# Kernel tuning notes

Measured on AMD Instinct MI355X. Metric: run time of the kernel, lower is better.

## Reference

```python
import jax, jax.numpy as jnp
import numpy as np

EPS = 1e-6     # vnn repo EPS used in VN nonlinearity / batchnorm norm
BN_EPS = 1e-5  # torch BatchNorm default eps
K = 40         # args.n_knn


def knn_idx(x, k):
    # x: (B, 3, N) -> (B, N, k) indices of k nearest neighbors (incl. self)
    inner = -2.0 * jnp.einsum('bdn,bdm->bnm', x, x)
    xx = jnp.sum(x * x, axis=1)  # (B, N)
    neg_dist = -xx[:, :, None] - inner - xx[:, None, :]
    _, idx = jax.lax.top_k(neg_dist, k)
    return idx


def get_graph_feature_cross(x, k):
    # x: (B, 3, N) -> (B, 3, 3, N, k): channels are [nbr - ctr, ctr, cross(nbr, ctr)]
    pts = jnp.transpose(x, (0, 2, 1))  # (B, N, 3)
    idx = knn_idx(x, k)                # (B, N, k)
    nbr = jax.vmap(lambda p, i: p[i])(pts, idx)          # (B, N, k, 3)
    ctr = jnp.broadcast_to(pts[:, :, None, :], nbr.shape)
    cross = jnp.cross(nbr, ctr)
    feat = jnp.stack([nbr - ctr, ctr, cross], axis=3)    # (B, N, k, 3, 3)
    return jnp.transpose(feat, (0, 3, 4, 1, 2))          # (B, C=3, 3vec, N, k)


def vn_bn(x):
    # VNBatchNorm (training-mode batch stats, affine = identity at init)
    # x: (B, C, 3, *rest); normalize the per-vector norm across (B, *rest)
    norm = jnp.sqrt(jnp.sum(x * x, axis=2)) + EPS  # (B, C, *rest)
    axes = (0,) + tuple(range(2, norm.ndim))
    mean = jnp.mean(norm, axis=axes, keepdims=True)
    var = jnp.var(norm, axis=axes, keepdims=True)
    norm_bn = (norm - mean) / jnp.sqrt(var + BN_EPS)
    return x / jnp.expand_dims(norm, 2) * jnp.expand_dims(norm_bn, 2)


def vn_lin(W, x):
    # channel-wise linear on axis 1 of (B, C, 3, ...)
    return jnp.einsum('oc,bc...->bo...', W, x)


def vn_lrelu(x, Wf, Wd):
    # VNLinearLeakyReLU with negative_slope=0.0
    p = vn_bn(vn_lin(Wf, x))
    d = vn_lin(Wd, x)
    dot = jnp.sum(p * d, axis=2, keepdims=True)
    dsq = jnp.sum(d * d, axis=2, keepdims=True)
    neg = p - (dot / (dsq + EPS)) * d  # project out the d component
    return jnp.where(dot >= 0, p, neg)


def vn_max_pool(x, W):
    # pool over last axis, picking the element maximizing <x, d> per (B, C, n)
    d = vn_lin(W, x)
    dot = jnp.sum(x * d, axis=2, keepdims=True)          # (B, C, 1, ..., K)
    idx = jnp.argmax(dot, axis=-1, keepdims=True)        # (B, C, 1, ..., 1)
    idx = jnp.broadcast_to(idx, x.shape[:-1] + (1,))
    return jnp.take_along_axis(x, idx, axis=-1)[..., 0]


def setup_inputs() -> dict:
    key = jax.random.key(0)
    ks = jax.random.split(key, 16)
    def w(k, o, i):
        bound = 1.0 / np.sqrt(i)  # torch nn.Linear default init
        return jax.random.uniform(k, (o, i), jnp.float32, -bound, bound)
    B, N = 8, 2048
    C1, C2, C3 = 64 // 3, 128 // 3, 1024 // 3  # 21, 42, 341
    F1, F2 = 512 // 3, 256 // 3                # 170, 85
    return {
        'x': jax.random.normal(ks[0], (B, 3, N), jnp.float32),
        'W_pos_feat': w(ks[1], C1, 3), 'W_pos_dir': w(ks[2], C1, 3),
        'W_gpool': w(ks[3], C1, C1),
        'W1_feat': w(ks[4], C1, C1), 'W1_dir': w(ks[5], C1, C1),
        'W2_feat': w(ks[6], C2, C1), 'W2_dir': w(ks[7], C2, C1),
        'W3_feat': w(ks[8], C3, C2), 'W3_dir': w(ks[9], C3, C2),
        'W_pool': w(ks[10], C3, C3),
        'Wf1_feat': w(ks[11], F1, C3), 'Wf1_dir': w(ks[12], F1, C3),
        'Wf2_feat': w(ks[13], F2, F1), 'Wf2_dir': w(ks[14], F2, F1),
        'Wf3': w(ks[15], 3, F2),
    }


def reference(x, W_pos_feat, W_pos_dir, W_gpool, W1_feat, W1_dir, W2_feat, W2_dir,
              W3_feat, W3_dir, W_pool, Wf1_feat, Wf1_dir, Wf2_feat, Wf2_dir, Wf3):
    feat = get_graph_feature_cross(x, K)            # (B, 3, 3, N, K)
    h = vn_lrelu(feat, W_pos_feat, W_pos_dir)       # (B, 21, 3, N, K)
    h = vn_max_pool(h, W_gpool)                     # (B, 21, 3, N)
    h = vn_lrelu(h, W1_feat, W1_dir)                # (B, 21, 3, N)
    h = vn_lrelu(h, W2_feat, W2_dir)                # (B, 42, 3, N)
    h = vn_lrelu(h, W3_feat, W3_dir)                # (B, 341, 3, N)
    h = vn_max_pool(h, W_pool)                      # (B, 341, 3)
    h = vn_lrelu(h, Wf1_feat, Wf1_dir)              # (B, 170, 3)
    h = vn_lrelu(h, Wf2_feat, Wf2_dir)              # (B, 85, 3)
    return vn_lin(Wf3, h)                           # (B, 3, 3)
```

## Files before the change

kernel.cpp:

```cpp
#include <hip/hip_runtime.h>

#define NP 2048
#define BATCH 8
#define KNN 40
#define EPSF 1e-6f
#define BNEPS 1e-5f

typedef __attribute__((ext_vector_type(8))) short short8;
typedef __attribute__((ext_vector_type(4))) float f32x4;

__device__ __forceinline__ unsigned ordf(float v){
  unsigned u = __float_as_uint(v);
  return (u & 0x80000000u) ? ~u : (u | 0x80000000u);
}

__device__ __forceinline__ void bsplit(float v, unsigned short &h, unsigned short &l){
  unsigned u = __float_as_uint(v);
  unsigned hu = (u + 0x7fffu + ((u >> 16) & 1u)) >> 16;
  h = (unsigned short)hu;
  float r = v - __uint_as_float(hu << 16);
  unsigned u2 = __float_as_uint(r);
  l = (unsigned short)((u2 + 0x7fffu + ((u2 >> 16) & 1u)) >> 16);
}

__device__ __forceinline__ float bf2f(unsigned short h){
  return __uint_as_float(((unsigned)h) << 16);
}

__global__ __launch_bounds__(256) void knn_kernel(const float* __restrict__ x, int* __restrict__ idx){
  __shared__ float4 sP[NP];
  int tid = threadIdx.x;
  int w = tid >> 6, lane = tid & 63;
  int row = blockIdx.x * 4 + w;
  int b = row >> 11, i = row & 2047;
  const float* xb = x + b * 3 * NP;
  for (int t = tid; t < NP; t += 256){
    float a = xb[t], c = xb[NP + t], d = xb[2*NP + t];
    float xx = __fadd_rn(__fadd_rn(__fmul_rn(a,a), __fmul_rn(c,c)), __fmul_rn(d,d));
    sP[t] = make_float4(a, c, d, xx);
  }
  __syncthreads();
  float4 pi = sP[i];
  const float4* lp = &sP[lane];
  unsigned long long s0 = 0, s1 = 0, s2 = 0, s3 = 0;
  #pragma unroll
  for (int m = 0; m < 32; m++){
    float4 pj = lp[m * 64];
    float dot = __fadd_rn(__fadd_rn(__fmul_rn(pi.x, pj.x), __fmul_rn(pi.y, pj.y)), __fmul_rn(pi.z, pj.z));
    float v = __fsub_rn(__fsub_rn(-pi.w, __fmul_rn(-2.f, dot)), pj.w);
    unsigned long long pk = ((unsigned long long)ordf(v) << 32) | (unsigned)(2047 - (m*64 + lane));
    if (pk > s3){
      if (pk > s2){ s3 = s2; if (pk > s1){ s2 = s1; if (pk > s0){ s1 = s0; s0 = pk; } else s1 = pk; } else s2 = pk; }
      else s3 = pk;
    }
  }
  unsigned myout = 0;
  unsigned long long lastPop = ~0ull;
  for (int kk = 0; kk < KNN; kk++){
    unsigned hv = (unsigned)(s0 >> 32);
    unsigned vm = hv;
    #pragma unroll
    for (int st = 32; st > 0; st >>= 1){
      unsigned o = (unsigned)__shfl_xor((int)vm, st, 64);
      vm = (o > vm) ? o : vm;
    }
    bool cand = (hv == vm);
    unsigned long long msk = __ballot(cand);
    unsigned lo;
    if (__popcll(msk) == 1){
      int wl = __ffsll((unsigned long long)msk) - 1;
      lo = (unsigned)__shfl((int)(unsigned)s0, wl, 64);
    } else {
      unsigned cl = cand ? (unsigned)s0 : 0u;
      #pragma unroll
      for (int st = 32; st > 0; st >>= 1){
        unsigned o = (unsigned)__shfl_xor((int)cl, st, 64);
        cl = (o > cl) ? o : cl;
      }
      lo = cl;
    }
    if (lane == kk) myout = lo;
    if (cand && (unsigned)s0 == lo){
      lastPop = s0;
      s0 = s1; s1 = s2; s2 = s3; s3 = 0;
      if (s0 == 0){
        unsigned long long best = 0;
        #pragma unroll
        for (int m = 0; m < 32; m++){
          float4 pj = lp[m * 64];
          float dot = __fadd_rn(__fadd_rn(__fmul_rn(pi.x, pj.x), __fmul_rn(pi.y, pj.y)), __fmul_rn(pi.z, pj.z));
          float v = __fsub_rn(__fsub_rn(-pi.w, __fmul_rn(-2.f, dot)), pj.w);
          unsigned long long pk = ((unsigned long long)ordf(v) << 32) | (unsigned)(2047 - (m*64 + lane));
          if (pk < lastPop && pk > best) best = pk;
        }
        s0 = best;
      }
    }
  }
  if (lane < KNN) idx[row * KNN + lane] = 2047 - (int)myout;
}

__global__ __launch_bounds__(256) void gf_stats(const float* __restrict__ x, const int* __restrict__ idx,
                                                const float* __restrict__ Wf, double* __restrict__ sums){
  int tid0 = blockIdx.x * 256 + threadIdx.x;
  float s[21], q[21];
  #pragma unroll
  for (int o = 0; o < 21; o++){ s[o] = 0.f; q[o] = 0.f; }
  for (int pix = tid0; pix < BATCH * NP * KNN; pix += 256 * 256){
    int rem = pix / KNN;
    int n = rem & 2047, b = rem >> 11;
    int j = idx[pix];
    const float* xb = x + b * 3 * NP;
    float c0 = xb[n], c1 = xb[NP + n], c2 = xb[2*NP + n];
    float a0 = xb[j], a1 = xb[NP + j], a2 = xb[2*NP + j];
    float r0 = a0 - c0, r1 = a1 - c1, r2 = a2 - c2;
    float g0 = a1*c2 - a2*c1, g1 = a2*c0 - a0*c2, g2 = a0*c1 - a1*c0;
    #pragma unroll
    for (int o = 0; o < 21; o++){
      float w0 = Wf[o*3], w1 = Wf[o*3+1], w2 = Wf[o*3+2];
      float p0 = w0*r0 + w1*c0 + w2*g0;
      float p1 = w0*r1 + w1*c1 + w2*g1;
      float p2 = w0*r2 + w1*c2 + w2*g2;
      float nm = sqrtf(p0*p0 + p1*p1 + p2*p2) + EPSF;
      s[o] += nm; q[o] += nm * nm;
    }
  }
  __shared__ float bs[4][42];
  int w = threadIdx.x >> 6;
  #pragma unroll
  for (int o = 0; o < 21; o++){
    float a = s[o], bb = q[o];
    #pragma unroll
    for (int st = 1; st < 64; st <<= 1){ a += __shfl_xor(a, st, 64); bb += __shfl_xor(bb, st, 64); }
    if ((threadIdx.x & 63) == 0){ bs[w][o] = a; bs[w][21 + o] = bb; }
  }
  __syncthreads();
  if (threadIdx.x < 42){
    float tot = bs[0][threadIdx.x] + bs[1][threadIdx.x] + bs[2][threadIdx.x] + bs[3][threadIdx.x];
    int o = threadIdx.x % 21, sq = threadIdx.x / 21;
    atomicAdd(&sums[2*o + sq], (double)tot);
  }
}

__global__ __launch_bounds__(256) void gf_applypool(const float* __restrict__ x, const int* __restrict__ idx,
    const float* __restrict__ Wf, const float* __restrict__ Wd, const float* __restrict__ Wg,
    const float* __restrict__ mi, float* __restrict__ h1){
  int w = threadIdx.x >> 6, lane = threadIdx.x & 63;
  int pix = blockIdx.x * 4 + w;
  int n = pix & 2047, b = pix >> 11;
  const float* xb = x + b * 3 * NP;
  float c0 = xb[n], c1 = xb[NP + n], c2 = xb[2*NP + n];
  int j = (lane < KNN) ? idx[pix * KNN + lane] : n;
  float a0 = xb[j], a1 = xb[NP + j], a2 = xb[2*NP + j];
  float r0 = a0 - c0, r1 = a1 - c1, r2 = a2 - c2;
  float g0 = a1*c2 - a2*c1, g1 = a2*c0 - a0*c2, g2 = a0*c1 - a1*c0;
  float h[21][3];
  #pragma unroll
  for (int o = 0; o < 21; o++){
    float w0 = Wf[o*3], w1 = Wf[o*3+1], w2 = Wf[o*3+2];
    float p0 = w0*r0 + w1*c0 + w2*g0;
    float p1 = w0*r1 + w1*c1 + w2*g1;
    float p2 = w0*r2 + w1*c2 + w2*g2;
    float nm = sqrtf(p0*p0 + p1*p1 + p2*p2) + EPSF;
    float f = (nm - mi[2*o]) * mi[2*o+1] / nm;
    p0 *= f; p1 *= f; p2 *= f;
    float v0 = Wd[o*3], v1 = Wd[o*3+1], v2 = Wd[o*3+2];
    float d0 = v0*r0 + v1*c0 + v2*g0;
    float d1 = v0*r1 + v1*c1 + v2*g1;
    float d2 = v0*r2 + v1*c2 + v2*g2;
    float dot = p0*d0 + p1*d1 + p2*d2;
    float dsq = d0*d0 + d1*d1 + d2*d2;
    float t = dot / (dsq + EPSF);
    h[o][0] = (dot >= 0.f) ? p0 : fmaf(-t, d0, p0);
    h[o][1] = (dot >= 0.f) ? p1 : fmaf(-t, d1, p1);
    h[o][2] = (dot >= 0.f) ? p2 : fmaf(-t, d2, p2);
  }
  #pragma unroll
  for (int o = 0; o < 21; o++){
    float q0 = 0.f, q1 = 0.f, q2 = 0.f;
    #pragma unroll
    for (int c = 0; c < 21; c++){
      float wg = Wg[o*21 + c];
      q0 = fmaf(wg, h[c][0], q0); q1 = fmaf(wg, h[c][1], q1); q2 = fmaf(wg, h[c][2], q2);
    }
    float dp = q0*h[o][0] + q1*h[o][1] + q2*h[o][2];
    float m = (lane < KNN) ? dp : -INFINITY;
    #pragma unroll
    for (int s = 32; s > 0; s >>= 1) m = fmaxf(m, __shfl_xor(m, s, 64));
    unsigned long long msk = __ballot(lane < KNN && dp == m);
    int wl = __ffsll(msk) - 1;
    float o0 = __shfl(h[o][0], wl, 64);
    float o1 = __shfl(h[o][1], wl, 64);
    float o2 = __shfl(h[o][2], wl, 64);
    if (lane == 0){
      float* dst = h1 + (size_t)((b*21 + o)*3) * NP + n;
      dst[0] = o0; dst[NP] = o1; dst[2*NP] = o2;
    }
  }
}

template<int CIN>
__global__ __launch_bounds__(256) void layer_stats2(const float* __restrict__ hin, const float* __restrict__ Wf,
                                                    double* __restrict__ sums, int Co){
  const int px0 = blockIdx.x * 1024;
  const int b = px0 >> 11;
  const int n0 = (px0 & 2047) + (threadIdx.x << 2);
  const int o0 = blockIdx.y * 8;
  const float* hb = hin + (size_t)b * CIN * 3 * NP + n0;
  float p[8][3][4];
  #pragma unroll
  for (int oo = 0; oo < 8; oo++)
    #pragma unroll
    for (int e = 0; e < 3; e++)
      #pragma unroll
      for (int k = 0; k < 4; k++) p[oo][e][k] = 0.f;
  for (int c = 0; c < CIN; c++){
    float4 hv[3];
    #pragma unroll
    for (int e = 0; e < 3; e++) hv[e] = *(const float4*)&hb[(size_t)(c*3 + e) * NP];
    #pragma unroll
    for (int oo = 0; oo < 8; oo++){
      int o = o0 + oo; if (o >= Co) o = Co - 1;
      float wv = Wf[o*CIN + c];
      #pragma unroll
      for (int e = 0; e < 3; e++){
        p[oo][e][0] = fmaf(wv, hv[e].x, p[oo][e][0]);
        p[oo][e][1] = fmaf(wv, hv[e].y, p[oo][e][1]);
        p[oo][e][2] = fmaf(wv, hv[e].z, p[oo][e][2]);
        p[oo][e][3] = fmaf(wv, hv[e].w, p[oo][e][3]);
      }
    }
  }
  float sl[8], ql[8];
  #pragma unroll
  for (int oo = 0; oo < 8; oo++){
    sl[oo] = 0.f; ql[oo] = 0.f;
    #pragma unroll
    for (int k = 0; k < 4; k++){
      float nm = sqrtf(p[oo][0][k]*p[oo][0][k] + p[oo][1][k]*p[oo][1][k] + p[oo][2][k]*p[oo][2][k]) + EPSF;
      sl[oo] += nm; ql[oo] += nm * nm;
    }
  }
  __shared__ float red[4][16];
  int w = threadIdx.x >> 6;
  #pragma unroll
  for (int oo = 0; oo < 8; oo++){
    float sv = sl[oo], qv = ql[oo];
    #pragma unroll
    for (int st = 1; st < 64; st <<= 1){ sv += __shfl_xor(sv, st, 64); qv += __shfl_xor(qv, st, 64); }
    if ((threadIdx.x & 63) == 0){ red[w][oo] = sv; red[w][8 + oo] = qv; }
  }
  __syncthreads();
  if (threadIdx.x < 16){
    float tot = red[0][threadIdx.x] + red[1][threadIdx.x] + red[2][threadIdx.x] + red[3][threadIdx.x];
    int oo = threadIdx.x & 7, isq = threadIdx.x >> 3;
    int o = o0 + oo;
    if (o < Co) atomicAdd(&sums[2*o + isq], (double)tot);
  }
}

template<int CIN>
__global__ __launch_bounds__(256) void layer_apply2(const float* __restrict__ hin, const float* __restrict__ Wf,
    const float* __restrict__ Wd, const float* __restrict__ mi, float* __restrict__ hout, int Co){
  const int px = blockIdx.x * 256 + threadIdx.x;
  const int b = px >> 11, n = px & 2047;
  const int o0 = blockIdx.y * 8;
  const float* hb = hin + (size_t)b * CIN * 3 * NP + n;
  float p[8][3], d[8][3];
  #pragma unroll
  for (int oo = 0; oo < 8; oo++)
    #pragma unroll
    for (int e = 0; e < 3; e++){ p[oo][e] = 0.f; d[oo][e] = 0.f; }
  for (int c = 0; c < CIN; c++){
    float h0 = hb[(size_t)(c*3 + 0) * NP];
    float h1 = hb[(size_t)(c*3 + 1) * NP];
    float h2 = hb[(size_t)(c*3 + 2) * NP];
    #pragma unroll
    for (int oo = 0; oo < 8; oo++){
      int o = o0 + oo; if (o >= Co) o = Co - 1;
      float wf = Wf[o*CIN + c], wd = Wd[o*CIN + c];
      p[oo][0] = fmaf(wf, h0, p[oo][0]); p[oo][1] = fmaf(wf, h1, p[oo][1]); p[oo][2] = fmaf(wf, h2, p[oo][2]);
      d[oo][0] = fmaf(wd, h0, d[oo][0]); d[oo][1] = fmaf(wd, h1, d[oo][1]); d[oo][2] = fmaf(wd, h2, d[oo][2]);
    }
  }
  #pragma unroll
  for (int oo = 0; oo < 8; oo++){
    int o = o0 + oo;
    if (o < Co){
      float nm = sqrtf(p[oo][0]*p[oo][0] + p[oo][1]*p[oo][1] + p[oo][2]*p[oo][2]) + EPSF;
      float f = (nm - mi[2*o]) * mi[2*o+1] / nm;
      float p0 = p[oo][0]*f, p1 = p[oo][1]*f, p2 = p[oo][2]*f;
      float dot = p0*d[oo][0] + p1*d[oo][1] + p2*d[oo][2];
      float dsq = d[oo][0]*d[oo][0] + d[oo][1]*d[oo][1] + d[oo][2]*d[oo][2];
      float t = dot / (dsq + EPSF);
      float r0 = (dot >= 0.f) ? p0 : fmaf(-t, d[oo][0], p0);
      float r1 = (dot >= 0.f) ? p1 : fmaf(-t, d[oo][1], p1);
      float r2 = (dot >= 0.f) ? p2 : fmaf(-t, d[oo][2], p2);
      float* dst = hout + (size_t)((b*Co + o)*3) * NP + n;
      dst[0] = r0; dst[NP] = r1; dst[2*NP] = r2;
    }
  }
}

__global__ __launch_bounds__(256) void layer_apply_l3v2(const float* __restrict__ hin, const float* __restrict__ Wf,
    const float* __restrict__ Wd, const float* __restrict__ mi,
    unsigned short* __restrict__ Hkh, unsigned short* __restrict__ Hkl){
  const int px = blockIdx.x * 256 + threadIdx.x;
  const int b = px >> 11, n = px & 2047;
  const int o0 = blockIdx.y * 8;
  const float* hb = hin + (size_t)b * 42 * 3 * NP + n;
  float r[8][3];
  #pragma unroll
  for (int oo = 0; oo < 8; oo++)
    #pragma unroll
    for (int e = 0; e < 3; e++) r[oo][e] = 0.f;
  if (o0 < 341){
    float p[8][3], d[8][3];
    #pragma unroll
    for (int oo = 0; oo < 8; oo++)
      #pragma unroll
      for (int e = 0; e < 3; e++){ p[oo][e] = 0.f; d[oo][e] = 0.f; }
    for (int c = 0; c < 42; c++){
      float h0 = hb[(size_t)(c*3 + 0) * NP];
      float h1 = hb[(size_t)(c*3 + 1) * NP];
      float h2 = hb[(size_t)(c*3 + 2) * NP];
      #pragma unroll
      for (int oo = 0; oo < 8; oo++){
        int o = o0 + oo; if (o >= 341) o = 340;
        float wf = Wf[o*42 + c], wd = Wd[o*42 + c];
        p[oo][0] = fmaf(wf, h0, p[oo][0]); p[oo][1] = fmaf(wf, h1, p[oo][1]); p[oo][2] = fmaf(wf, h2, p[oo][2]);
        d[oo][0] = fmaf(wd, h0, d[oo][0]); d[oo][1] = fmaf(wd, h1, d[oo][1]); d[oo][2] = fmaf(wd, h2, d[oo][2]);
      }
    }
    #pragma unroll
    for (int oo = 0; oo < 8; oo++){
      int o = o0 + oo;
      if (o < 341){
        float nm = sqrtf(p[oo][0]*p[oo][0] + p[oo][1]*p[oo][1] + p[oo][2]*p[oo][2]) + EPSF;
        float f = (nm - mi[2*o]) * mi[2*o+1] / nm;
        float p0 = p[oo][0]*f, p1 = p[oo][1]*f, p2 = p[oo][2]*f;
        float dot = p0*d[oo][0] + p1*d[oo][1] + p2*d[oo][2];
        float dsq = d[oo][0]*d[oo][0] + d[oo][1]*d[oo][1] + d[oo][2]*d[oo][2];
        float t = dot / (dsq + EPSF);
        r[oo][0] = (dot >= 0.f) ? p0 : fmaf(-t, d[oo][0], p0);
        r[oo][1] = (dot >= 0.f) ? p1 : fmaf(-t, d[oo][1], p1);
        r[oo][2] = (dot >= 0.f) ? p2 : fmaf(-t, d[oo][2], p2);
      }
    }
  }
  #pragma unroll
  for (int e = 0; e < 3; e++){
    unsigned ph[4], pl[4];
    #pragma unroll
    for (int oo = 0; oo < 8; oo++){
      unsigned short hh, ll;
      bsplit(r[oo][e], hh, ll);
      if (!(oo & 1)){ ph[oo>>1] = hh; pl[oo>>1] = ll; }
      else { ph[oo>>1] |= ((unsigned)hh) << 16; pl[oo>>1] |= ((unsigned)ll) << 16; }
    }
    size_t base = ((((size_t)(b*3 + e))*48 + blockIdx.y) * 2048 + n) * 8;
    *(uint4*)(Hkh + base) = make_uint4(ph[0], ph[1], ph[2], ph[3]);
    *(uint4*)(Hkl + base) = make_uint4(pl[0], pl[1], pl[2], pl[3]);
  }
}

__global__ void finalize_stats(const double* __restrict__ sums, float* __restrict__ mi, int Co, double invM){
  int o = blockIdx.x * 64 + threadIdx.x;
  if (o >= Co) return;
  double m = sums[2*o] * invM;
  double v = sums[2*o+1] * invM - m * m;
  if (v < 0.0) v = 0.0;
  mi[2*o] = (float)m;
  mi[2*o+1] = (float)(1.0 / sqrt(v + (double)BNEPS));
}

__global__ __launch_bounds__(256) void wk_kernel(const float* __restrict__ Wp,
    unsigned short* __restrict__ Wkh, unsigned short* __restrict__ Wkl){
  int t = blockIdx.x * 256 + threadIdx.x;
  if (t >= 44*384*8) return;
  int j = t & 7, o = (t >> 3) % 384, cb = t / (384*8);
  int c = cb*8 + j;
  float v = (c < 341 && o < 341) ? Wp[o*341 + c] : 0.f;
  unsigned short h, l;
  bsplit(v, h, l);
  Wkh[t] = h; Wkl[t] = l;
}

__global__ __launch_bounds__(256) void pool_mfma(const unsigned short* __restrict__ Wkh,
    const unsigned short* __restrict__ Wkl, const unsigned short* __restrict__ Hkh,
    const unsigned short* __restrict__ Hkl, unsigned long long* __restrict__ packed){
  __shared__ unsigned short sB[2][2][4][64][8];
  const int b = blockIdx.z, o0 = blockIdx.y * 128, n0 = blockIdx.x * 64;
  const int t = threadIdx.x, w = t >> 6, l = t & 63;
  const int wo = o0 + w * 32;
  const int r = l & 15, g = l >> 4;
  const int skb = t >> 6, sn = t & 63;
  const int ktw = wo >> 5;

  f32x4 acc[2][4], dotv[2][4], hval[2][4];
  #pragma unroll
  for (int s = 0; s < 2; s++)
    #pragma unroll
    for (int nt = 0; nt < 4; nt++){ dotv[s][nt] = (f32x4)0.f; hval[s][nt] = (f32x4)0.f; }

  auto gsrc = [&](const unsigned short* base, int e, int kt) -> const uint4* {
    return (const uint4*)(base + ((((size_t)(b*3 + e))*48 + (size_t)(kt*4 + skb)) * 2048 + n0 + sn) * 8);
  };

  uint4 rg[2];
  rg[0] = *gsrc(Hkh, 0, 0);
  rg[1] = *gsrc(Hkl, 0, 0);

  for (int ek = 0; ek < 33; ek++){
    const int e = ek / 11, kt = ek - e*11, buf = ek & 1;
    *(uint4*)&sB[buf][0][skb][sn][0] = rg[0];
    *(uint4*)&sB[buf][1][skb][sn][0] = rg[1];
    __syncthreads();
    if (ek < 32){
      int e2 = (ek+1) / 11, kt2 = (ek+1) - e2*11;
      rg[0] = *gsrc(Hkh, e2, kt2);
      rg[1] = *gsrc(Hkl, e2, kt2);
    }
    if (kt == 0){
      #pragma unroll
      for (int s = 0; s < 2; s++)
        #pragma unroll
        for (int nt = 0; nt < 4; nt++) acc[s][nt] = (f32x4)0.f;
    }
    short8 ah[2], al[2];
    #pragma unroll
    for (int s = 0; s < 2; s++){
      size_t aoff = (((size_t)(kt*4 + g)) * 384 + (wo + s*16 + r)) * 8;
      ah[s] = *(const short8*)(Wkh + aoff);
      al[s] = *(const short8*)(Wkl + aoff);
    }
    #pragma unroll
    for (int nt = 0; nt < 4; nt++){
      short8 bh = *(const short8*)&sB[buf][0][g][nt*16 + r][0];
      short8 bl = *(const short8*)&sB[buf][1][g][nt*16 + r][0];
      #pragma unroll
      for (int s = 0; s < 2; s++){
        acc[s][nt] = __builtin_amdgcn_mfma_f32_16x16x32_bf16(ah[s], bh, acc[s][nt], 0, 0, 0);
        acc[s][nt] = __builtin_amdgcn_mfma_f32_16x16x32_bf16(ah[s], bl, acc[s][nt], 0, 0, 0);
        acc[s][nt] = __builtin_amdgcn_mfma_f32_16x16x32_bf16(al[s], bh, acc[s][nt], 0, 0, 0);
      }
    }
    if (kt == ktw){
      #pragma unroll
      for (int s = 0; s < 2; s++){
        #pragma unroll
        for (int jj = 0; jj < 4; jj++){
          int oin = s*16 + g*4 + jj;
          #pragma unroll
          for (int nt = 0; nt < 4; nt++){
            hval[s][nt][jj] = bf2f(sB[buf][0][oin>>3][nt*16 + r][oin&7])
                            + bf2f(sB[buf][1][oin>>3][nt*16 + r][oin&7]);
          }
        }
      }
    }
    __syncthreads();
    if (kt == 10){
      #pragma unroll
      for (int s = 0; s < 2; s++)
        #pragma unroll
        for (int nt = 0; nt < 4; nt++)
          #pragma unroll
          for (int jj = 0; jj < 4; jj++)
            dotv[s][nt][jj] += acc[s][nt][jj] * hval[s][nt][jj];
    }
  }
  #pragma unroll
  for (int s = 0; s < 2; s++){
    #pragma unroll
    for (int j = 0; j < 4; j++){
      int o = wo + s*16 + g*4 + j;
      unsigned long long best = 0;
      #pragma unroll
      for (int nt = 0; nt < 4; nt++){
        int n = n0 + nt*16 + r;
        unsigned long long pk = ((unsigned long long)ordf(dotv[s][nt][j]) << 32) | (unsigned)(2047 - n);
        if (pk > best) best = pk;
      }
      #pragma unroll
      for (int st = 1; st < 16; st <<= 1){
        unsigned long long ob = __shfl_xor(best, st, 64);
        if (ob > best) best = ob;
      }
      if (r == 0 && o < 341) atomicMax(&packed[b*341 + o], best);
    }
  }
}

__global__ void pool_gather(const unsigned long long* __restrict__ packed,
                            const unsigned short* __restrict__ Hkh, const unsigned short* __restrict__ Hkl,
                            float* __restrict__ pooled){
  int t = blockIdx.x * 256 + threadIdx.x;
  if (t >= BATCH * 341) return;
  int n = 2047 - (int)(packed[t] & 0xffffffffu);
  int b = t / 341, o = t % 341;
  #pragma unroll
  for (int e = 0; e < 3; e++){
    size_t hb = ((((size_t)(b*3 + e))*48 + (o >> 3)) * 2048 + n) * 8 + (o & 7);
    pooled[t*3 + e] = bf2f(Hkh[hb]) + bf2f(Hkl[hb]);
  }
}

__global__ __launch_bounds__(64) void flayer(const float* __restrict__ in, const float* __restrict__ Wf,
    const float* __restrict__ Wd, float* __restrict__ out, int Cin, int Co){
  int o = blockIdx.x, lane = threadIdx.x;
  float pv[24], dv[24];
  #pragma unroll
  for (int be = 0; be < 24; be++){ pv[be] = 0.f; dv[be] = 0.f; }
  for (int c = lane; c < Cin; c += 64){
    float wf = Wf[o*Cin + c], wd = Wd[o*Cin + c];
    #pragma unroll
    for (int bb = 0; bb < 8; bb++){
      #pragma unroll
      for (int e = 0; e < 3; e++){
        float hv = in[(bb*Cin + c)*3 + e];
        pv[bb*3+e] = fmaf(wf, hv, pv[bb*3+e]);
        dv[bb*3+e] = fmaf(wd, hv, dv[bb*3+e]);
      }
    }
  }
  #pragma unroll
  for (int be = 0; be < 24; be++){
    #pragma unroll
    for (int st = 1; st < 64; st <<= 1){
      pv[be] += __shfl_xor(pv[be], st, 64);
      dv[be] += __shfl_xor(dv[be], st, 64);
    }
  }
  float nm[8], dotb[8], dsqb[8];
  float mean = 0.f;
  #pragma unroll
  for (int bb = 0; bb < 8; bb++){
    nm[bb] = sqrtf(pv[bb*3]*pv[bb*3] + pv[bb*3+1]*pv[bb*3+1] + pv[bb*3+2]*pv[bb*3+2]) + EPSF;
    mean += nm[bb];
  }
  mean *= 0.125f;
  float var = 0.f;
  #pragma unroll
  for (int bb = 0; bb < 8; bb++){ float dvv = nm[bb] - mean; var += dvv * dvv; }
  var *= 0.125f;
  float istd = 1.f / sqrtf(var + BNEPS);
  #pragma unroll
  for (int bb = 0; bb < 8; bb++){
    float f = (nm[bb] - mean) * istd / nm[bb];
    dotb[bb] = f * (pv[bb*3]*dv[bb*3] + pv[bb*3+1]*dv[bb*3+1] + pv[bb*3+2]*dv[bb*3+2]);
    dsqb[bb] = dv[bb*3]*dv[bb*3] + dv[bb*3+1]*dv[bb*3+1] + dv[bb*3+2]*dv[bb*3+2];
  }
  #pragma unroll
  for (int be = 0; be < 24; be++){
    if (lane == be){
      int bb = be / 3;
      float f = (nm[bb] - mean) * istd / nm[bb];
      float pe = pv[be] * f;
      float t = dotb[bb] / (dsqb[bb] + EPSF);
      float res = (dotb[bb] >= 0.f) ? pe : fmaf(-t, dv[be], pe);
      out[(bb*Co + o)*3 + (be % 3)] = res;
    }
  }
}

__global__ void final_lin(const float* __restrict__ in, const float* __restrict__ W, float* __restrict__ out){
  int t = threadIdx.x;
  if (t >= 72) return;
  int b = t / 9, o = (t % 9) / 3, e = t % 3;
  float s = 0.f;
  for (int c = 0; c < 85; c++) s = fmaf(W[o*85 + c], in[(b*85 + c)*3 + e], s);
  out[t] = s;
}

extern "C" void kernel_launch(void* const* d_in, const int* in_sizes, int n_in,
                              void* d_out, int out_size, void* d_ws, size_t ws_size,
                              hipStream_t stream){
  const float* x   = (const float*)d_in[0];
  const float* Wpf = (const float*)d_in[1];
  const float* Wpd = (const float*)d_in[2];
  const float* Wg  = (const float*)d_in[3];
  const float* W1f = (const float*)d_in[4];
  const float* W1d = (const float*)d_in[5];
  const float* W2f = (const float*)d_in[6];
  const float* W2d = (const float*)d_in[7];
  const float* W3f = (const float*)d_in[8];
  const float* W3d = (const float*)d_in[9];
  const float* Wpool = (const float*)d_in[10];
  const float* Wf1f = (const float*)d_in[11];
  const float* Wf1d = (const float*)d_in[12];
  const float* Wf2f = (const float*)d_in[13];
  const float* Wf2d = (const float*)d_in[14];
  const float* Wf3  = (const float*)d_in[15];
  float* out = (float*)d_out;

  char* ws = (char*)d_ws;
  size_t off = 0;
  int*   idx = (int*)(ws + off);              off += (size_t)BATCH*NP*KNN*4;
  float* h1  = (float*)(ws + off);            off += (size_t)BATCH*21*3*NP*4;
  float* h2  = (float*)(ws + off);            off += (size_t)BATCH*21*3*NP*4;
  float* h3  = (float*)(ws + off);            off += (size_t)BATCH*42*3*NP*4;
  unsigned short* Hkh = (unsigned short*)(ws + off); off += (size_t)BATCH*3*48*NP*8*2;
  unsigned short* Hkl = (unsigned short*)(ws + off); off += (size_t)BATCH*3*48*NP*8*2;
  unsigned short* Wkh = (unsigned short*)(ws + off); off += (size_t)44*384*8*2;
  unsigned short* Wkl = (unsigned short*)(ws + off); off += (size_t)44*384*8*2;
  char*  zbase = ws + off;
  double* sums_gf = (double*)(ws + off);      off += 8192;
  double* sums_l1 = (double*)(ws + off);      off += 8192;
  double* sums_l2 = (double*)(ws + off);      off += 8192;
  double* sums_l3 = (double*)(ws + off);      off += 8192;
  unsigned long long* packed = (unsigned long long*)(ws + off); off += 24576;
  size_t zbytes = (ws + off) - zbase;
  float* mi_gf = (float*)(ws + off);          off += 1024;
  float* mi_l1 = (float*)(ws + off);          off += 1024;
  float* mi_l2 = (float*)(ws + off);          off += 1024;
  float* mi_l3 = (float*)(ws + off);          off += 4096;
  float* pooled = (float*)(ws + off);         off += (size_t)BATCH*341*3*4 + 32;
  float* h5 = (float*)(ws + off);             off += (size_t)BATCH*170*3*4 + 32;
  float* h6 = (float*)(ws + off);             off += (size_t)BATCH*85*3*4 + 32;

  hipMemsetAsync(zbase, 0, zbytes, stream);

  knn_kernel<<<BATCH*NP/4, 256, 0, stream>>>(x, idx);
  wk_kernel<<<(44*384*8 + 255)/256, 256, 0, stream>>>(Wpool, Wkh, Wkl);

  gf_stats<<<256, 256, 0, stream>>>(x, idx, Wpf, sums_gf);
  finalize_stats<<<1, 64, 0, stream>>>(sums_gf, mi_gf, 21, 1.0 / (double)(BATCH*NP*KNN));
  gf_applypool<<<BATCH*NP/4, 256, 0, stream>>>(x, idx, Wpf, Wpd, Wg, mi_gf, h1);

  layer_stats2<21><<<dim3(16,3), 256, 0, stream>>>(h1, W1f, sums_l1, 21);
  finalize_stats<<<1, 64, 0, stream>>>(sums_l1, mi_l1, 21, 1.0 / (double)(BATCH*NP));
  layer_apply2<21><<<dim3(64,3), 256, 0, stream>>>(h1, W1f, W1d, mi_l1, h2, 21);

  layer_stats2<21><<<dim3(16,6), 256, 0, stream>>>(h2, W2f, sums_l2, 42);
  finalize_stats<<<1, 64, 0, stream>>>(sums_l2, mi_l2, 42, 1.0 / (double)(BATCH*NP));
  layer_apply2<21><<<dim3(64,6), 256, 0, stream>>>(h2, W2f, W2d, mi_l2, h3, 42);

  layer_stats2<42><<<dim3(16,43), 256, 0, stream>>>(h3, W3f, sums_l3, 341);
  finalize_stats<<<6, 64, 0, stream>>>(sums_l3, mi_l3, 341, 1.0 / (double)(BATCH*NP));
  layer_apply_l3v2<<<dim3(64,44), 256, 0, stream>>>(h3, W3f, W3d, mi_l3, Hkh, Hkl);

  pool_mfma<<<dim3(32, 3, BATCH), 256, 0, stream>>>(Wkh, Wkl, Hkh, Hkl, packed);
  pool_gather<<<(BATCH*341 + 255)/256, 256, 0, stream>>>(packed, Hkh, Hkl, pooled);

  flayer<<<170, 64, 0, stream>>>(pooled, Wf1f, Wf1d, h5, 341, 170);
  flayer<<<85, 64, 0, stream>>>(h5, Wf2f, Wf2d, h6, 170, 85);
  final_lin<<<1, 128, 0, stream>>>(h6, Wf3, out);
}
```

Before: 533.6 us.

## Restructure first-layer apply+pool to 8 threads per point with packed argmax

The first VN layer plus max-pool kernel is remapped from one wavefront per point (40 of 64 lanes active) to 8 threads per point, each handling 5 neighbours. Each thread keeps a packed (score, index) running max per channel, and the winners are reduced with three xor shuffles. Afterwards the winning neighbour's feature is recomputed rather than shuffled across lanes. This removes the idle lanes and the per-channel 64-wide reductions, at the cost of a second, transposed index array written by the knn kernel and extra recompute work per output.

```diff
diff --git a/kernel.cpp b/kernel.cpp
--- a/kernel.cpp
+++ b/kernel.cpp
@@ -27,7 +27,8 @@
   return __uint_as_float(((unsigned)h) << 16);
 }
 
-__global__ __launch_bounds__(256) void knn_kernel(const float* __restrict__ x, int* __restrict__ idx){
+__global__ __launch_bounds__(256) void knn_kernel(const float* __restrict__ x, int* __restrict__ idx,
+                                                  int* __restrict__ idxT){
   __shared__ float4 sP[NP];
   int tid = threadIdx.x;
   int w = tid >> 6, lane = tid & 63;
@@ -97,7 +98,11 @@
       }
     }
   }
-  if (lane < KNN) idx[row * KNN + lane] = 2047 - (int)myout;
+  if (lane < KNN){
+    int v = 2047 - (int)myout;
+    idx[row * KNN + lane] = v;
+    idxT[lane * (BATCH*NP) + row] = v;
+  }
 }
 
 __global__ __launch_bounds__(256) void gf_stats(const float* __restrict__ x, const int* __restrict__ idx,
@@ -142,57 +147,99 @@
   }
 }
 
-__global__ __launch_bounds__(256) void gf_applypool(const float* __restrict__ x, const int* __restrict__ idx,
+#define KSPLIT 8
+#define KPER 5
+__global__ __launch_bounds__(256) void gf_applypool2(const float* __restrict__ x, const int* __restrict__ idxT,
     const float* __restrict__ Wf, const float* __restrict__ Wd, const float* __restrict__ Wg,
     const float* __restrict__ mi, float* __restrict__ h1){
-  int w = threadIdx.x >> 6, lane = threadIdx.x & 63;
-  int pix = blockIdx.x * 4 + w;
-  int n = pix & 2047, b = pix >> 11;
+  __shared__ float4 sP[NP];
+  const int tid = threadIdx.x;
+  const int pxl = tid >> 3, kc = tid & 7;
+  const int px = blockIdx.x * 32 + pxl;
+  const int b = px >> 11, n = px & 2047;
   const float* xb = x + b * 3 * NP;
-  float c0 = xb[n], c1 = xb[NP + n], c2 = xb[2*NP + n];
-  int j = (lane < KNN) ? idx[pix * KNN + lane] : n;
-  float a0 = xb[j], a1 = xb[NP + j], a2 = xb[2*NP + j];
-  float r0 = a0 - c0, r1 = a1 - c1, r2 = a2 - c2;
-  float g0 = a1*c2 - a2*c1, g1 = a2*c0 - a0*c2, g2 = a0*c1 - a1*c0;
-  float h[21][3];
+  for (int t = tid; t < NP; t += 256){
+    sP[t] = make_float4(xb[t], xb[NP + t], xb[2*NP + t], 0.f);
+  }
+  __syncthreads();
+  float4 pc = sP[n];
+  unsigned long long bestpk[21];
+  #pragma unroll
+  for (int o = 0; o < 21; o++) bestpk[o] = 0ull;
+  #pragma unroll 1
+  for (int ki = 0; ki < KPER; ki++){
+    int kg = kc * KPER + ki;
+    int j = idxT[kg * (BATCH*NP) + px];
+    float4 pj = sP[j];
+    float r0 = pj.x - pc.x, r1 = pj.y - pc.y, r2 = pj.z - pc.z;
+    float g0 = pj.y*pc.z - pj.z*pc.y, g1 = pj.z*pc.x - pj.x*pc.z, g2 = pj.x*pc.y - pj.y*pc.x;
+    float h[21][3];
+    #pragma unroll
+    for (int o = 0; o < 21; o++){
+      float w0 = Wf[o*3], w1 = Wf[o*3+1], w2 = Wf[o*3+2];
+      float p0 = w0*r0 + w1*pc.x + w2*g0;
+      float p1 = w0*r1 + w1*pc.y + w2*g1;
+      float p2 = w0*r2 + w1*pc.z + w2*g2;
+      float nm = sqrtf(p0*p0 + p1*p1 + p2*p2) + EPSF;
+      float f = (nm - mi[2*o]) * mi[2*o+1] / nm;
+      p0 *= f; p1 *= f; p2 *= f;
+      float v0 = Wd[o*3], v1 = Wd[o*3+1], v2 = Wd[o*3+2];
+      float d0 = v0*r0 + v1*pc.x + v2*g0;
+      float d1 = v0*r1 + v1*pc.y + v2*g1;
+      float d2 = v0*r2 + v1*pc.z + v2*g2;
+      float dot = p0*d0 + p1*d1 + p2*d2;
+      float dsq = d0*d0 + d1*d1 + d2*d2;
+      float t = dot / (dsq + EPSF);
+      h[o][0] = (dot >= 0.f) ? p0 : fmaf(-t, d0, p0);
+      h[o][1] = (dot >= 0.f) ? p1 : fmaf(-t, d1, p1);
+      h[o][2] = (dot >= 0.f) ? p2 : fmaf(-t, d2, p2);
+    }
+    #pragma unroll
+    for (int o = 0; o < 21; o++){
+      float q0 = 0.f, q1 = 0.f, q2 = 0.f;
+      #pragma unroll
+      for (int c = 0; c < 21; c++){
+        float wg = Wg[o*21 + c];
+        q0 = fmaf(wg, h[c][0], q0); q1 = fmaf(wg, h[c][1], q1); q2 = fmaf(wg, h[c][2], q2);
+      }
+      float dp = q0*h[o][0] + q1*h[o][1] + q2*h[o][2];
+      unsigned long long pk = ((unsigned long long)ordf(dp) << 32) | (unsigned)(63 - kg);
+      if (pk > bestpk[o]) bestpk[o] = pk;
+    }
+  }
   #pragma unroll
   for (int o = 0; o < 21; o++){
+    unsigned long long v = bestpk[o];
+    unsigned long long t = __shfl_xor(v, 1, 64); if (t > v) v = t;
+    t = __shfl_xor(v, 2, 64); if (t > v) v = t;
+    t = __shfl_xor(v, 4, 64); if (t > v) v = t;
+    bestpk[o] = v;
+  }
+  #pragma unroll
+  for (int o = 0; o < 21; o++){
+    int kst = 63 - (int)(bestpk[o] & 0xffffffffu);
+    int j = idxT[kst * (BATCH*NP) + px];
+    float4 pj = sP[j];
+    float r0 = pj.x - pc.x, r1 = pj.y - pc.y, r2 = pj.z - pc.z;
+    float g0 = pj.y*pc.z - pj.z*pc.y, g1 = pj.z*pc.x - pj.x*pc.z, g2 = pj.x*pc.y - pj.y*pc.x;
     float w0 = Wf[o*3], w1 = Wf[o*3+1], w2 = Wf[o*3+2];
-    float p0 = w0*r0 + w1*c0 + w2*g0;
-    float p1 = w0*r1 + w1*c1 + w2*g1;
-    float p2 = w0*r2 + w1*c2 + w2*g2;
+    float p0 = w0*r0 + w1*pc.x + w2*g0;
+    float p1 = w0*r1 + w1*pc.y + w2*g1;
+    float p2 = w0*r2 + w1*pc.z + w2*g2;
     float nm = sqrtf(p0*p0 + p1*p1 + p2*p2) + EPSF;
     float f = (nm - mi[2*o]) * mi[2*o+1] / nm;
     p0 *= f; p1 *= f; p2 *= f;
     float v0 = Wd[o*3], v1 = Wd[o*3+1], v2 = Wd[o*3+2];
-    float d0 = v0*r0 + v1*c0 + v2*g0;
-    float d1 = v0*r1 + v1*c1 + v2*g1;
-    float d2 = v0*r2 + v1*c2 + v2*g2;
+    float d0 = v0*r0 + v1*pc.x + v2*g0;
+    float d1 = v0*r1 + v1*pc.y + v2*g1;
+    float d2 = v0*r2 + v1*pc.z + v2*g2;
     float dot = p0*d0 + p1*d1 + p2*d2;
     float dsq = d0*d0 + d1*d1 + d2*d2;
     float t = dot / (dsq + EPSF);
-    h[o][0] = (dot >= 0.f) ? p0 : fmaf(-t, d0, p0);
-    h[o][1] = (dot >= 0.f) ? p1 : fmaf(-t, d1, p1);
-    h[o][2] = (dot >= 0.f) ? p2 : fmaf(-t, d2, p2);
-  }
-  #pragma unroll
-  for (int o = 0; o < 21; o++){
-    float q0 = 0.f, q1 = 0.f, q2 = 0.f;
-    #pragma unroll
-    for (int c = 0; c < 21; c++){
-      float wg = Wg[o*21 + c];
-      q0 = fmaf(wg, h[c][0], q0); q1 = fmaf(wg, h[c][1], q1); q2 = fmaf(wg, h[c][2], q2);
-    }
-    float dp = q0*h[o][0] + q1*h[o][1] + q2*h[o][2];
-    float m = (lane < KNN) ? dp : -INFINITY;
-    #pragma unroll
-    for (int s = 32; s > 0; s >>= 1) m = fmaxf(m, __shfl_xor(m, s, 64));
-    unsigned long long msk = __ballot(lane < KNN && dp == m);
-    int wl = __ffsll(msk) - 1;
-    float o0 = __shfl(h[o][0], wl, 64);
-    float o1 = __shfl(h[o][1], wl, 64);
-    float o2 = __shfl(h[o][2], wl, 64);
-    if (lane == 0){
+    float o0 = (dot >= 0.f) ? p0 : fmaf(-t, d0, p0);
+    float o1 = (dot >= 0.f) ? p1 : fmaf(-t, d1, p1);
+    float o2 = (dot >= 0.f) ? p2 : fmaf(-t, d2, p2);
+    if (kc == 0){
       float* dst = h1 + (size_t)((b*21 + o)*3) * NP + n;
       dst[0] = o0; dst[NP] = o1; dst[2*NP] = o2;
     }
@@ -596,7 +643,8 @@
 
   char* ws = (char*)d_ws;
   size_t off = 0;
-  int*   idx = (int*)(ws + off);              off += (size_t)BATCH*NP*KNN*4;
+  int*   idx  = (int*)(ws + off);             off += (size_t)BATCH*NP*KNN*4;
+  int*   idxT = (int*)(ws + off);             off += (size_t)BATCH*NP*KNN*4;
   float* h1  = (float*)(ws + off);            off += (size_t)BATCH*21*3*NP*4;
   float* h2  = (float*)(ws + off);            off += (size_t)BATCH*21*3*NP*4;
   float* h3  = (float*)(ws + off);            off += (size_t)BATCH*42*3*NP*4;
@@ -621,12 +669,12 @@
 
   hipMemsetAsync(zbase, 0, zbytes, stream);
 
-  knn_kernel<<<BATCH*NP/4, 256, 0, stream>>>(x, idx);
+  knn_kernel<<<BATCH*NP/4, 256, 0, stream>>>(x, idx, idxT);
   wk_kernel<<<(44*384*8 + 255)/256, 256, 0, stream>>>(Wpool, Wkh, Wkl);
 
   gf_stats<<<256, 256, 0, stream>>>(x, idx, Wpf, sums_gf);
   finalize_stats<<<1, 64, 0, stream>>>(sums_gf, mi_gf, 21, 1.0 / (double)(BATCH*NP*KNN));
-  gf_applypool<<<BATCH*NP/4, 256, 0, stream>>>(x, idx, Wpf, Wpd, Wg, mi_gf, h1);
+  gf_applypool2<<<BATCH*NP/32, 256, 0, stream>>>(x, idxT, Wpf, Wpd, Wg, mi_gf, h1);
 
   layer_stats2<21><<<dim3(16,3), 256, 0, stream>>>(h1, W1f, sums_l1, 21);
   finalize_stats<<<1, 64, 0, stream>>>(sums_l1, mi_l1, 21, 1.0 / (double)(BATCH*NP));
```

After: 628.7 us. 1.18x slower.

## Pack neighbor lanes densely and use shared atomicMax argmax with separate gather kernel

Applied to the files above, without the earlier changes.

The first-layer apply+pool kernel used one 64-lane wavefront per point with only 40 active lanes. It now packs 8 points into a 320-thread block so every lane is busy. The per-channel argmax moves from shuffle reductions to packed 64-bit shared-memory atomicMax keys. A new gather kernel recomputes the winning neighbor's activation and writes h1. This adds an extra launch, a packed index buffer, and a small amount of recomputation, and the first-index tie-breaking is kept by encoding 63-k.

```diff
diff --git a/kernel.cpp b/kernel.cpp
--- a/kernel.cpp
+++ b/kernel.cpp
@@ -142,15 +142,19 @@
   }
 }
 
-__global__ __launch_bounds__(256) void gf_applypool(const float* __restrict__ x, const int* __restrict__ idx,
+__global__ __launch_bounds__(320) void gf_applypool3(const float* __restrict__ x, const int* __restrict__ idx,
     const float* __restrict__ Wf, const float* __restrict__ Wd, const float* __restrict__ Wg,
-    const float* __restrict__ mi, float* __restrict__ h1){
-  int w = threadIdx.x >> 6, lane = threadIdx.x & 63;
-  int pix = blockIdx.x * 4 + w;
-  int n = pix & 2047, b = pix >> 11;
+    const float* __restrict__ mi, unsigned long long* __restrict__ packedGF){
+  __shared__ unsigned long long sM[8*21];
+  const int tid = threadIdx.x;
+  for (int t = tid; t < 168; t += 320) sM[t] = 0ull;
+  __syncthreads();
+  const int pxl = tid / 40, k = tid - pxl * 40;
+  const int px = blockIdx.x * 8 + pxl;
+  const int b = px >> 11, n = px & 2047;
   const float* xb = x + b * 3 * NP;
   float c0 = xb[n], c1 = xb[NP + n], c2 = xb[2*NP + n];
-  int j = (lane < KNN) ? idx[pix * KNN + lane] : n;
+  int j = idx[(size_t)px * KNN + k];
   float a0 = xb[j], a1 = xb[NP + j], a2 = xb[2*NP + j];
   float r0 = a0 - c0, r1 = a1 - c1, r2 = a2 - c2;
   float g0 = a1*c2 - a2*c1, g1 = a2*c0 - a0*c2, g2 = a0*c1 - a1*c0;
@@ -184,19 +188,49 @@
       q0 = fmaf(wg, h[c][0], q0); q1 = fmaf(wg, h[c][1], q1); q2 = fmaf(wg, h[c][2], q2);
     }
     float dp = q0*h[o][0] + q1*h[o][1] + q2*h[o][2];
-    float m = (lane < KNN) ? dp : -INFINITY;
-    #pragma unroll
-    for (int s = 32; s > 0; s >>= 1) m = fmaxf(m, __shfl_xor(m, s, 64));
-    unsigned long long msk = __ballot(lane < KNN && dp == m);
-    int wl = __ffsll(msk) - 1;
-    float o0 = __shfl(h[o][0], wl, 64);
-    float o1 = __shfl(h[o][1], wl, 64);
-    float o2 = __shfl(h[o][2], wl, 64);
-    if (lane == 0){
-      float* dst = h1 + (size_t)((b*21 + o)*3) * NP + n;
-      dst[0] = o0; dst[NP] = o1; dst[2*NP] = o2;
-    }
-  }
+    unsigned long long pk = ((unsigned long long)ordf(dp) << 32) | (unsigned)(63 - k);
+    atomicMax(&sM[pxl*21 + o], pk);
+  }
+  __syncthreads();
+  for (int t = tid; t < 168; t += 320){
+    int lpx = t / 21, lo = t - lpx * 21;
+    packedGF[(size_t)(blockIdx.x * 8 + lpx) * 21 + lo] = sM[t];
+  }
+}
+
+__global__ __launch_bounds__(256) void gf_gather(const float* __restrict__ x, const int* __restrict__ idx,
+    const float* __restrict__ Wf, const float* __restrict__ Wd, const float* __restrict__ mi,
+    const unsigned long long* __restrict__ packedGF, float* __restrict__ h1){
+  int t = blockIdx.x * 256 + threadIdx.x;
+  if (t >= BATCH * NP * 21) return;
+  int px = t / 21, o = t - px * 21;
+  int b = px >> 11, n = px & 2047;
+  int k = 63 - (int)(packedGF[t] & 0xffffffffu);
+  int j = idx[(size_t)px * KNN + k];
+  const float* xb = x + b * 3 * NP;
+  float c0 = xb[n], c1 = xb[NP + n], c2 = xb[2*NP + n];
+  float a0 = xb[j], a1 = xb[NP + j], a2 = xb[2*NP + j];
+  float r0 = a0 - c0, r1 = a1 - c1, r2 = a2 - c2;
+  float g0 = a1*c2 - a2*c1, g1 = a2*c0 - a0*c2, g2 = a0*c1 - a1*c0;
+  float w0 = Wf[o*3], w1 = Wf[o*3+1], w2 = Wf[o*3+2];
+  float p0 = w0*r0 + w1*c0 + w2*g0;
+  float p1 = w0*r1 + w1*c1 + w2*g1;
+  float p2 = w0*r2 + w1*c2 + w2*g2;
+  float nm = sqrtf(p0*p0 + p1*p1 + p2*p2) + EPSF;
+  float f = (nm - mi[2*o]) * mi[2*o+1] / nm;
+  p0 *= f; p1 *= f; p2 *= f;
+  float v0 = Wd[o*3], v1 = Wd[o*3+1], v2 = Wd[o*3+2];
+  float d0 = v0*r0 + v1*c0 + v2*g0;
+  float d1 = v0*r1 + v1*c1 + v2*g1;
+  float d2 = v0*r2 + v1*c2 + v2*g2;
+  float dot = p0*d0 + p1*d1 + p2*d2;
+  float dsq = d0*d0 + d1*d1 + d2*d2;
+  float tt = dot / (dsq + EPSF);
+  float o0 = (dot >= 0.f) ? p0 : fmaf(-tt, d0, p0);
+  float o1 = (dot >= 0.f) ? p1 : fmaf(-tt, d1, p1);
+  float o2 = (dot >= 0.f) ? p2 : fmaf(-tt, d2, p2);
+  float* dst = h1 + (size_t)((b*21 + o)*3) * NP + n;
+  dst[0] = o0; dst[NP] = o1; dst[2*NP] = o2;
 }
 
 template<int CIN>
@@ -596,7 +630,8 @@
 
   char* ws = (char*)d_ws;
   size_t off = 0;
-  int*   idx = (int*)(ws + off);              off += (size_t)BATCH*NP*KNN*4;
+  int*   idx  = (int*)(ws + off);             off += (size_t)BATCH*NP*KNN*4;
+  unsigned long long* packedGF = (unsigned long long*)(ws + off); off += (size_t)BATCH*NP*21*8;
   float* h1  = (float*)(ws + off);            off += (size_t)BATCH*21*3*NP*4;
   float* h2  = (float*)(ws + off);            off += (size_t)BATCH*21*3*NP*4;
   float* h3  = (float*)(ws + off);            off += (size_t)BATCH*42*3*NP*4;
@@ -626,7 +661,8 @@
 
   gf_stats<<<256, 256, 0, stream>>>(x, idx, Wpf, sums_gf);
   finalize_stats<<<1, 64, 0, stream>>>(sums_gf, mi_gf, 21, 1.0 / (double)(BATCH*NP*KNN));
-  gf_applypool<<<BATCH*NP/4, 256, 0, stream>>>(x, idx, Wpf, Wpd, Wg, mi_gf, h1);
+  gf_applypool3<<<BATCH*NP/8, 320, 0, stream>>>(x, idx, Wpf, Wpd, Wg, mi_gf, packedGF);
+  gf_gather<<<(BATCH*NP*21 + 255)/256, 256, 0, stream>>>(x, idx, Wpf, Wpd, mi_gf, packedGF, h1);
 
   layer_stats2<21><<<dim3(16,3), 256, 0, stream>>>(h1, W1f, sums_l1, 21);
   finalize_stats<<<1, 64, 0, stream>>>(sums_l1, mi_l1, 21, 1.0 / (double)(BATCH*NP));
```

After: 507.3 us. -4.9%, faster.
